# Kernel tuning notes

Hardware: AMD Instinct MI355X
Metric: run time of the kernel (lower is better)

The kernel has to match this reference:

```python
import jax, jax.numpy as jnp
import numpy as np


def fps(xyz, npoint):
    # farthest point sampling, starts at index 0 (matches pointnet2 CUDA kernel)
    B, N, _ = xyz.shape
    def step(carry, _):
        min_d, last = carry
        last_xyz = jnp.take_along_axis(xyz, last[:, None, None], axis=1)  # [B,1,3]
        d = jnp.sum((xyz - last_xyz) ** 2, axis=-1)                        # [B,N]
        min_d = jnp.minimum(min_d, d)
        nxt = jnp.argmax(min_d, axis=1).astype(jnp.int32)
        return (min_d, nxt), last
    init = (jnp.full((B, N), 1e10, xyz.dtype), jnp.zeros((B,), jnp.int32))
    _, idx = jax.lax.scan(step, init, None, length=npoint)
    return jnp.transpose(idx)  # [B, npoint]


def ball_query(xyz, new_xyz, radius, nsample):
    # first nsample points within radius; pad with first hit (0 if none) -- CUDA semantics
    N = xyz.shape[1]
    d2 = jnp.sum((new_xyz[:, :, None, :] - xyz[:, None, :, :]) ** 2, axis=-1)  # [B,S,N]
    cand = jnp.where(d2 < radius * radius, jnp.arange(N, dtype=jnp.int32)[None, None, :], N)
    srt = jnp.sort(cand, axis=-1)[..., :nsample]
    first = srt[..., :1]
    first = jnp.where(first == N, 0, first)
    return jnp.where(srt == N, first, srt)  # [B,S,K]


def gather_nbrs(x, idx):
    # x [B,N,C], idx [B,S,K] -> [B,S,K,C]
    B, S, K = idx.shape
    flat = jnp.take_along_axis(x, idx.reshape(B, S * K, 1), axis=1)
    return flat.reshape(B, S, K, x.shape[-1])


def shared_mlp(x, layers):
    # 1x1 conv (+ folded eval-mode BN) + ReLU per layer
    for w, b in layers:
        x = jax.nn.relu(jnp.einsum('bskc,oc->bsko', x, w) + b)
    return x


def sa_module(xyz, feat, npoint, radius, nsample, layers):
    idx = fps(xyz, npoint)
    new_xyz = jnp.take_along_axis(xyz, idx[:, :, None], axis=1)  # [B,S,3]
    gidx = ball_query(xyz, new_xyz, radius, nsample)
    grouped = gather_nbrs(xyz, gidx) - new_xyz[:, :, None, :]    # centered local xyz
    if feat is not None:
        grouped = jnp.concatenate([grouped, gather_nbrs(feat, gidx)], axis=-1)
    x = shared_mlp(grouped, layers)
    return new_xyz, jnp.max(x, axis=2)  # max-pool over neighbors -> [B,S,Cout]


def sa_module_all(xyz, feat, layers):
    # GroupAll: concat raw (uncentered) xyz with features, one group of all points
    x = jnp.concatenate([xyz, feat], axis=-1)[:, None]  # [B,1,N,3+C]
    x = shared_mlp(x, layers)
    return jnp.max(x, axis=2)[:, 0]  # [B,Cout]


def _forward(data, ws):
    B, T, N, _ = data.shape
    xyz = data.reshape(B * T, N, 3)
    xyz, feat = sa_module(xyz, None, 256, 0.2, 32, ws[0])
    xyz, feat = sa_module(xyz, feat, 128, 0.4, 32, ws[1])
    out = sa_module_all(xyz, feat, ws[2])
    return out.reshape(B, T, -1)


DIMS = [(3, 64), (64, 64), (64, 128), (131, 128), (128, 128), (128, 256), (259, 256), (256, 512), (512, 1024)]
NAMES = ['1_0', '1_1', '1_2', '2_0', '2_1', '2_2', '3_0', '3_1', '3_2']


def setup_inputs() -> dict:
    key = jax.random.key(0)
    keys = jax.random.split(key, 1 + 2 * len(DIMS))
    inp = {'data': jax.random.normal(keys[0], (4, 8, 4096, 3), jnp.float32)}
    for i, ((cin, cout), nm) in enumerate(zip(DIMS, NAMES)):
        inp['w' + nm] = jax.random.normal(keys[1 + 2 * i], (cout, cin), jnp.float32) / np.sqrt(cin).astype(np.float32)
        inp['b' + nm] = jax.random.normal(keys[2 + 2 * i], (cout,), jnp.float32) * 0.02
    return inp


def reference(data, w1_0, b1_0, w1_1, b1_1, w1_2, b1_2,
              w2_0, b2_0, w2_1, b2_1, w2_2, b2_2,
              w3_0, b3_0, w3_1, b3_1, w3_2, b3_2):
    ws = [[(w1_0, b1_0), (w1_1, b1_1), (w1_2, b1_2)],
          [(w2_0, b2_0), (w2_1, b2_1), (w2_2, b2_2)],
          [(w3_0, b3_0), (w3_1, b3_1), (w3_2, b3_2)]]
    return _forward(data, ws)
```

## Files before the change

kernel.cpp:

```cpp
#include <hip/hip_runtime.h>
#include <hip/hip_bf16.h>
#include <cstdint>
#include <cstddef>

#define BT 32
#define N1 4096
#define S1 256
#define S2 128
#define KNB 32

typedef __attribute__((ext_vector_type(8))) short short8;
typedef __attribute__((ext_vector_type(4))) float f32x4;

__device__ __forceinline__ float sqdist(float ax, float ay, float az,
                                        float bx, float by, float bz) {
    float dx = __fsub_rn(ax, bx), dy = __fsub_rn(ay, by), dz = __fsub_rn(az, bz);
    return __fadd_rn(__fadd_rn(__fmul_rn(dx, dx), __fmul_rn(dy, dy)), __fmul_rn(dz, dz));
}

__device__ __forceinline__ unsigned short f2bf(float f) {
    unsigned u = __float_as_uint(f);
    return (unsigned short)((u + 0x7FFFu + ((u >> 16) & 1u)) >> 16);
}
__device__ __forceinline__ float bf2f(unsigned short h) {
    return __uint_as_float(((unsigned)h) << 16);
}

__device__ __forceinline__ unsigned long long packvi(float v, int idx) {
    return ((unsigned long long)__float_as_uint(v) << 32) | (unsigned)(~idx);
}

template <int CTRL>
__device__ __forceinline__ unsigned long long dppmax(unsigned long long v) {
    int lo = (int)(unsigned)(v & 0xFFFFFFFFull);
    int hi = (int)(unsigned)(v >> 32);
    int lo2 = __builtin_amdgcn_update_dpp(0, lo, CTRL, 0xF, 0xF, false);
    int hi2 = __builtin_amdgcn_update_dpp(0, hi, CTRL, 0xF, 0xF, false);
    unsigned long long o = ((unsigned long long)(unsigned)hi2 << 32) | (unsigned)lo2;
    return o > v ? o : v;
}
#define ROR1 0x121
#define ROR2 0x122
#define ROR4 0x124
#define ROR8 0x128

__global__ __launch_bounds__(256) void fps1_kernel(const float* __restrict__ xyz,
                                                   float* __restrict__ nxz) {
    const int b = blockIdx.x, tid = threadIdx.x;
    const int lane = tid & 63, wv = tid >> 6;
    const float* X = xyz + (size_t)b * (N1 * 3);
    __shared__ float4 s4[N1];
    __shared__ unsigned long long slots[2][16];
    __shared__ float hist[S1 * 3];
    float px[16], py[16], pz[16], md[16];
    int bidx[16];
#pragma unroll
    for (int j = 0; j < 16; ++j) {
        int i = tid + 256 * j;
        float x = X[i * 3 + 0], y = X[i * 3 + 1], z = X[i * 3 + 2];
        s4[i] = make_float4(x, y, z, 0.f);
        px[j] = x; py[j] = y; pz[j] = z;
        md[j] = 1e10f;
        bidx[j] = i;
    }
    if (tid == 0) { hist[0] = X[0]; hist[1] = X[1]; hist[2] = X[2]; }
    __syncthreads();
    float4 c0 = s4[0];
    float lx = c0.x, ly = c0.y, lz = c0.z;
    for (int t = 1; t < S1; ++t) {
        float bv = -1.0f; int bi = 0;
#pragma unroll
        for (int j = 0; j < 16; ++j) {
            float d = sqdist(px[j], py[j], pz[j], lx, ly, lz);
            float m = fminf(md[j], d);
            md[j] = m;
            if (m > bv) { bv = m; bi = bidx[j]; }
        }
        unsigned long long best = packvi(bv, bi);
        best = dppmax<ROR1>(best);
        best = dppmax<ROR2>(best);
        best = dppmax<ROR4>(best);
        best = dppmax<ROR8>(best);
        if ((lane & 15) == 0) slots[t & 1][wv * 4 + (lane >> 4)] = best;
        __syncthreads();
        unsigned long long w = slots[t & 1][lane & 15];
        w = dppmax<ROR1>(w);
        w = dppmax<ROR2>(w);
        w = dppmax<ROR4>(w);
        w = dppmax<ROR8>(w);
        int vi = (int)(~(unsigned)w);
        float4 c = s4[vi];
        lx = c.x; ly = c.y; lz = c.z;
        if (tid == 0) { hist[t * 3 + 0] = lx; hist[t * 3 + 1] = ly; hist[t * 3 + 2] = lz; }
    }
    __syncthreads();
    for (int u = tid; u < S1 * 3; u += 256) nxz[(size_t)b * S1 * 3 + u] = hist[u];
}

__global__ __launch_bounds__(64) void fps2_kernel(const float* __restrict__ xyz1,
                                                  float* __restrict__ nxz2) {
    const int b = blockIdx.x, lane = threadIdx.x;
    const float* X = xyz1 + (size_t)b * (S1 * 3);
    __shared__ float4 s4[S1];
    float px[4], py[4], pz[4], md[4];
    int bidx[4];
#pragma unroll
    for (int j = 0; j < 4; ++j) {
        int i = lane + 64 * j;
        float x = X[i * 3 + 0], y = X[i * 3 + 1], z = X[i * 3 + 2];
        s4[i] = make_float4(x, y, z, 0.f);
        px[j] = x; py[j] = y; pz[j] = z;
        md[j] = 1e10f;
        bidx[j] = i;
    }
    if (lane == 0) {
        nxz2[(size_t)b * S2 * 3 + 0] = X[0];
        nxz2[(size_t)b * S2 * 3 + 1] = X[1];
        nxz2[(size_t)b * S2 * 3 + 2] = X[2];
    }
    float4 cc = s4[0];
    float lx = cc.x, ly = cc.y, lz = cc.z;
    for (int t = 1; t < S2; ++t) {
        float bv = -1.0f; int bi = 0;
#pragma unroll
        for (int j = 0; j < 4; ++j) {
            float d = sqdist(px[j], py[j], pz[j], lx, ly, lz);
            float m = fminf(md[j], d);
            md[j] = m;
            if (m > bv) { bv = m; bi = bidx[j]; }
        }
        unsigned long long best = packvi(bv, bi);
        best = dppmax<ROR1>(best);
        best = dppmax<ROR2>(best);
        best = dppmax<ROR4>(best);
        best = dppmax<ROR8>(best);
        { unsigned long long o = __shfl_xor(best, 16); best = o > best ? o : best; }
        { unsigned long long o = __shfl_xor(best, 32); best = o > best ? o : best; }
        int vi = (int)(~(unsigned)best);
        float4 c = s4[vi];
        lx = c.x; ly = c.y; lz = c.z;
        if (lane == 0) {
            float* dst = nxz2 + ((size_t)b * S2 + t) * 3;
            dst[0] = lx; dst[1] = ly; dst[2] = lz;
        }
    }
}

__global__ __launch_bounds__(256) void ballq1_kernel(const float* __restrict__ xyz,
                                                     const float* __restrict__ nxz,
                                                     int* __restrict__ gidx) {
    const int wid = (blockIdx.x * 256 + threadIdx.x) >> 6;
    const int lane = threadIdx.x & 63;
    const int b = wid >> 8;
    const float* X = xyz + (size_t)b * (N1 * 3);
    const float* C = nxz + (size_t)wid * 3;
    const float cx = C[0], cy = C[1], cz = C[2];
    const float r2 = (float)(0.2 * 0.2);
    int* G = gidx + (size_t)wid * KNB;
    int cnt = 0, first = 0;
    bool found = false;
    for (int j0 = 0; j0 < N1 && cnt < KNB; j0 += 64) {
        int j = j0 + lane;
        float d2 = sqdist(cx, cy, cz, X[j * 3 + 0], X[j * 3 + 1], X[j * 3 + 2]);
        bool hit = d2 < r2;
        unsigned long long mask = __ballot(hit);
        if (!found && mask) { first = j0 + __builtin_ctzll(mask); found = true; }
        if (hit) {
            int pos = cnt + __popcll(mask & ((1ull << lane) - 1ull));
            if (pos < KNB) G[pos] = j;
        }
        cnt += __popcll(mask);
    }
    if (cnt < KNB) {
        int pad = found ? first : 0;
        if (lane >= cnt && lane < KNB) G[lane] = pad;
    }
}

__global__ __launch_bounds__(256) void ballq2_kernel(const float* __restrict__ xyz1,
                                                     const float* __restrict__ nxz2,
                                                     int* __restrict__ gidx) {
    const int wid = (blockIdx.x * 256 + threadIdx.x) >> 6;
    const int lane = threadIdx.x & 63;
    const int b = wid >> 7;
    const float* X = xyz1 + (size_t)b * (S1 * 3);
    const float* C = nxz2 + (size_t)wid * 3;
    const float cx = C[0], cy = C[1], cz = C[2];
    const float r2 = (float)(0.4 * 0.4);
    int* G = gidx + (size_t)wid * KNB;
    int cnt = 0, first = 0;
    bool found = false;
    for (int j0 = 0; j0 < S1 && cnt < KNB; j0 += 64) {
        int j = j0 + lane;
        float d2 = sqdist(cx, cy, cz, X[j * 3 + 0], X[j * 3 + 1], X[j * 3 + 2]);
        bool hit = d2 < r2;
        unsigned long long mask = __ballot(hit);
        if (!found && mask) { first = j0 + __builtin_ctzll(mask); found = true; }
        if (hit) {
            int pos = cnt + __popcll(mask & ((1ull << lane) - 1ull));
            if (pos < KNB) G[pos] = j;
        }
        cnt += __popcll(mask);
    }
    if (cnt < KNB) {
        int pad = found ? first : 0;
        if (lane >= cnt && lane < KNB) G[lane] = pad;
    }
}

__global__ __launch_bounds__(256) void wconv_kernel(
    const float* __restrict__ w11, const float* __restrict__ w12,
    const float* __restrict__ w20, const float* __restrict__ w21,
    const float* __restrict__ w22, const float* __restrict__ w30,
    const float* __restrict__ w31, const float* __restrict__ w32,
    unsigned short* __restrict__ wb) {
    int u = blockIdx.x * 256 + threadIdx.x;
    if (u >= 823296) return;
    const float* src; int base, Kp, Ko; int perm = 0;
    if      (u < 4096)   { src = w11; base = 0;      Kp = 64;  Ko = 64;  }
    else if (u < 12288)  { src = w12; base = 4096;   Kp = 64;  Ko = 64;  }
    else if (u < 36864)  { src = w20; base = 12288;  Kp = 192; Ko = 131; perm = 128; }
    else if (u < 53248)  { src = w21; base = 36864;  Kp = 128; Ko = 128; }
    else if (u < 86016)  { src = w22; base = 53248;  Kp = 128; Ko = 128; }
    else if (u < 167936) { src = w30; base = 86016;  Kp = 320; Ko = 259; perm = 256; }
    else if (u < 299008) { src = w31; base = 167936; Kp = 256; Ko = 256; }
    else                 { src = w32; base = 299008; Kp = 512; Ko = 512; }
    int local = u - base;
    int n = local / Kp, k = local - n * Kp;
    float v;
    if (perm) {
        int ksrc = (k < perm) ? (k + 3) : ((k < perm + 3) ? (k - perm) : -1);
        v = (ksrc >= 0) ? src[(size_t)n * Ko + ksrc] : 0.f;
    } else {
        v = (k < Ko) ? src[(size_t)n * Ko + k] : 0.f;
    }
    wb[u] = f2bf(v);
}

__global__ __launch_bounds__(256) void m1_kernel(
    const float* __restrict__ xyz, const float* __restrict__ nxz,
    const int* __restrict__ g1,
    const float* __restrict__ w10, const float* __restrict__ b10,
    const unsigned short* __restrict__ w11b, const float* __restrict__ b11,
    const unsigned short* __restrict__ w12b, const float* __restrict__ b12,
    unsigned short* __restrict__ f1) {
    constexpr int AP = 72;
    __shared__ __align__(16) unsigned short As[128 * AP];
    __shared__ __align__(16) unsigned short Hs[128 * AP];
    __shared__ __align__(16) unsigned short Bs[128 * AP];
    __shared__ float sxyz[128 * 3];
    const int t = threadIdx.x;
    const int lane = t & 63, w = t >> 6;
    const int r16 = lane & 15, q = lane >> 4;
    const int m0 = blockIdx.x * 128;

    if (t < 128) {
        int row = m0 + t, bs = row >> 5, b = bs >> 8, j = g1[row];
        const float* P = xyz + ((size_t)b * N1 + j) * 3;
        const float* Cc = nxz + (size_t)bs * 3;
        sxyz[t * 3 + 0] = P[0] - Cc[0];
        sxyz[t * 3 + 1] = P[1] - Cc[1];
        sxyz[t * 3 + 2] = P[2] - Cc[2];
    }
    for (int c = t; c < 64 * 8; c += 256) {
        int row = c >> 3, ch = c & 7;
        *(short8*)&Bs[row * AP + ch * 8] = *(const short8*)&w11b[row * 64 + ch * 8];
    }
    __syncthreads();
    {
        const int r = t >> 1, half = (t & 1) * 32;
        const float x = sxyz[r * 3 + 0], y = sxyz[r * 3 + 1], z = sxyz[r * 3 + 2];
        unsigned short tmp[32];
#pragma unroll
        for (int o = 0; o < 32; ++o) {
            int oo = half + o;
            float acc = b10[oo];
            acc = fmaf(x, w10[oo * 3 + 0], acc);
            acc = fmaf(y, w10[oo * 3 + 1], acc);
            acc = fmaf(z, w10[oo * 3 + 2], acc);
            tmp[o] = f2bf(fmaxf(acc, 0.f));
        }
#pragma unroll
        for (int c2 = 0; c2 < 4; ++c2)
            *(short8*)&As[r * AP + half + c2 * 8] = *(short8*)&tmp[c2 * 8];
    }
    __syncthreads();
    {
        f32x4 acc[2][4];
#pragma unroll
        for (int i = 0; i < 2; ++i)
#pragma unroll
            for (int j = 0; j < 4; ++j) acc[i][j] = (f32x4){0.f, 0.f, 0.f, 0.f};
#pragma unroll
        for (int kk = 0; kk < 64; kk += 32) {
            short8 a0 = *(const short8*)&As[(w * 32 + r16) * AP + kk + q * 8];
            short8 a1 = *(const short8*)&As[(w * 32 + 16 + r16) * AP + kk + q * 8];
#pragma unroll
            for (int j = 0; j < 4; ++j) {
                short8 bf = *(const short8*)&Bs[(j * 16 + r16) * AP + kk + q * 8];
                acc[0][j] = __builtin_amdgcn_mfma_f32_16x16x32_bf16(a0, bf, acc[0][j], 0, 0, 0);
                acc[1][j] = __builtin_amdgcn_mfma_f32_16x16x32_bf16(a1, bf, acc[1][j], 0, 0, 0);
            }
        }
#pragma unroll
        for (int i = 0; i < 2; ++i)
#pragma unroll
            for (int j = 0; j < 4; ++j) {
                int col = j * 16 + r16;
                float bv = b11[col];
#pragma unroll
                for (int r = 0; r < 4; ++r) {
                    int row = w * 32 + i * 16 + q * 4 + r;
                    Hs[row * AP + col] = f2bf(fmaxf(acc[i][j][r] + bv, 0.f));
                }
            }
    }
    __syncthreads();
    for (int c = t; c < 128 * 8; c += 256) {
        int row = c >> 3, ch = c & 7;
        *(short8*)&Bs[row * AP + ch * 8] = *(const short8*)&w12b[row * 64 + ch * 8];
    }
    __syncthreads();
    {
        f32x4 acc[2][8];
#pragma unroll
        for (int i = 0; i < 2; ++i)
#pragma unroll
            for (int j = 0; j < 8; ++j) acc[i][j] = (f32x4){0.f, 0.f, 0.f, 0.f};
#pragma unroll
        for (int kk = 0; kk < 64; kk += 32) {
            short8 a0 = *(const short8*)&Hs[(w * 32 + r16) * AP + kk + q * 8];
            short8 a1 = *(const short8*)&Hs[(w * 32 + 16 + r16) * AP + kk + q * 8];
#pragma unroll
            for (int j = 0; j < 8; ++j) {
                short8 bf = *(const short8*)&Bs[(j * 16 + r16) * AP + kk + q * 8];
                acc[0][j] = __builtin_amdgcn_mfma_f32_16x16x32_bf16(a0, bf, acc[0][j], 0, 0, 0);
                acc[1][j] = __builtin_amdgcn_mfma_f32_16x16x32_bf16(a1, bf, acc[1][j], 0, 0, 0);
            }
        }
#pragma unroll
        for (int j = 0; j < 8; ++j) {
            int col = j * 16 + r16;
            float bv = b12[col];
            float mv = 0.f;
#pragma unroll
            for (int i = 0; i < 2; ++i)
#pragma unroll
                for (int r = 0; r < 4; ++r)
                    mv = fmaxf(mv, acc[i][j][r] + bv);
            mv = fmaxf(mv, __shfl_xor(mv, 16));
            mv = fmaxf(mv, __shfl_xor(mv, 32));
            if (q == 0)
                f1[(size_t)((m0 >> 5) + w) * 128 + col] = f2bf(mv);
        }
    }
}

__global__ __launch_bounds__(256) void m2_kernel(
    const float* __restrict__ xyz1, const float* __restrict__ nxz2,
    const int* __restrict__ g2, const unsigned short* __restrict__ f1,
    const unsigned short* __restrict__ w20p, const float* __restrict__ b20,
    const unsigned short* __restrict__ w21b, const float* __restrict__ b21,
    const unsigned short* __restrict__ w22b, const float* __restrict__ b22,
    unsigned short* __restrict__ f2) {
    constexpr int AP = 72, HP = 136;
    __shared__ __align__(16) unsigned short smem[36864];
    unsigned short* R1 = smem;
    unsigned short* R2 = smem + 18432;
    unsigned short* As = R1;
    unsigned short* Bs = R1 + 9216;
    unsigned short* H1 = R2;
    unsigned short* H2 = R1;
    unsigned short* Bs2 = R2;
    __shared__ int ribase[128];
    __shared__ unsigned short sxb[128 * 3];
    const int t = threadIdx.x;
    const int lane = t & 63, w = t >> 6;
    const int r16 = lane & 15, q = lane >> 4;
    const int m0 = blockIdx.x * 128;

    if (t < 128) {
        int row = m0 + t, bs = row >> 5, b = bs >> 7, j = g2[row];
        ribase[t] = (b * 256 + j) * 128;
        const float* P = xyz1 + ((size_t)b * S1 + j) * 3;
        const float* Cc = nxz2 + (size_t)bs * 3;
        sxb[t * 3 + 0] = f2bf(P[0] - Cc[0]);
        sxb[t * 3 + 1] = f2bf(P[1] - Cc[1]);
        sxb[t * 3 + 2] = f2bf(P[2] - Cc[2]);
    }
    __syncthreads();

    f32x4 acc[2][8];
#pragma unroll
    for (int i = 0; i < 2; ++i)
#pragma unroll
        for (int j = 0; j < 8; ++j) acc[i][j] = (f32x4){0.f, 0.f, 0.f, 0.f};
    for (int kt = 0; kt < 3; ++kt) {
        const int k0 = kt * 64;
        if (kt < 2) {
            for (int c = t; c < 128 * 8; c += 256) {
                int row = c >> 3, ch = c & 7;
                *(short8*)&As[row * AP + ch * 8] =
                    *(const short8*)&f1[(size_t)ribase[row] + k0 + ch * 8];
            }
        } else {
            for (int c = t; c < 128 * 8; c += 256) {
                int row = c >> 3, ch = c & 7;
                short8 v = (short8){0, 0, 0, 0, 0, 0, 0, 0};
                if (ch == 0) {
                    v[0] = (short)sxb[row * 3 + 0];
                    v[1] = (short)sxb[row * 3 + 1];
                    v[2] = (short)sxb[row * 3 + 2];
                }
                *(short8*)&As[row * AP + ch * 8] = v;
            }
        }
        for (int c = t; c < 128 * 8; c += 256) {
            int row = c >> 3, ch = c & 7;
            *(short8*)&Bs[row * AP + ch * 8] =
                *(const short8*)&w20p[(size_t)row * 192 + k0 + ch * 8];
        }
        __syncthreads();
#pragma unroll
        for (int kk = 0; kk < 64; kk += 32) {
            short8 a0 = *(const short8*)&As[(w * 32 + r16) * AP + kk + q * 8];
            short8 a1 = *(const short8*)&As[(w * 32 + 16 + r16) * AP + kk + q * 8];
#pragma unroll
            for (int j = 0; j < 8; ++j) {
                short8 bf = *(const short8*)&Bs[(j * 16 + r16) * AP + kk + q * 8];
                acc[0][j] = __builtin_amdgcn_mfma_f32_16x16x32_bf16(a0, bf, acc[0][j], 0, 0, 0);
                acc[1][j] = __builtin_amdgcn_mfma_f32_16x16x32_bf16(a1, bf, acc[1][j], 0, 0, 0);
            }
        }
        __syncthreads();
    }
#pragma unroll
    for (int i = 0; i < 2; ++i)
#pragma unroll
        for (int j = 0; j < 8; ++j) {
            int col = j * 16 + r16;
            float bv = b20[col];
#pragma unroll
            for (int r = 0; r < 4; ++r) {
                int row = w * 32 + i * 16 + q * 4 + r;
                H1[row * HP + col] = f2bf(fmaxf(acc[i][j][r] + bv, 0.f));
            }
        }
    __syncthreads();

#pragma unroll
    for (int i = 0; i < 2; ++i)
#pragma unroll
        for (int j = 0; j < 8; ++j) acc[i][j] = (f32x4){0.f, 0.f, 0.f, 0.f};
    for (int kt = 0; kt < 2; ++kt) {
        const int k0 = kt * 64;
        for (int c = t; c < 128 * 8; c += 256) {
            int row = c >> 3, ch = c & 7;
            *(short8*)&As[row * AP + ch * 8] =
                *(const short8*)&w21b[(size_t)row * 128 + k0 + ch * 8];
        }
        __syncthreads();
#pragma unroll
        for (int kk = 0; kk < 64; kk += 32) {
            short8 a0 = *(const short8*)&H1[(w * 32 + r16) * HP + k0 + kk + q * 8];
            short8 a1 = *(const short8*)&H1[(w * 32 + 16 + r16) * HP + k0 + kk + q * 8];
#pragma unroll
            for (int j = 0; j < 8; ++j) {
                short8 bf = *(const short8*)&As[(j * 16 + r16) * AP + kk + q * 8];
                acc[0][j] = __builtin_amdgcn_mfma_f32_16x16x32_bf16(a0, bf, acc[0][j], 0, 0, 0);
                acc[1][j] = __builtin_amdgcn_mfma_f32_16x16x32_bf16(a1, bf, acc[1][j], 0, 0, 0);
            }
        }
        __syncthreads();
    }
#pragma unroll
    for (int i = 0; i < 2; ++i)
#pragma unroll
        for (int j = 0; j < 8; ++j) {
            int col = j * 16 + r16;
            float bv = b21[col];
#pragma unroll
            for (int r = 0; r < 4; ++r) {
                int row = w * 32 + i * 16 + q * 4 + r;
                H2[row * HP + col] = f2bf(fmaxf(acc[i][j][r] + bv, 0.f));
            }
        }
    __syncthreads();

    f32x4 acc2[2][16];
#pragma unroll
    for (int i = 0; i < 2; ++i)
#pragma unroll
        for (int j = 0; j < 16; ++j) acc2[i][j] = (f32x4){0.f, 0.f, 0.f, 0.f};
    for (int kt = 0; kt < 2; ++kt) {
        const int k0 = kt * 64;
        for (int c = t; c < 256 * 8; c += 256) {
            int row = c >> 3, ch = c & 7;
            *(short8*)&Bs2[row * AP + ch * 8] =
                *(const short8*)&w22b[(size_t)row * 128 + k0 + ch * 8];
        }
        __syncthreads();
#pragma unroll
        for (int kk = 0; kk < 64; kk += 32) {
            short8 a0 = *(const short8*)&H2[(w * 32 + r16) * HP + k0 + kk + q * 8];
            short8 a1 = *(const short8*)&H2[(w * 32 + 16 + r16) * HP + k0 + kk + q * 8];
#pragma unroll
            for (int j = 0; j < 16; ++j) {
                short8 bf = *(const short8*)&Bs2[(j * 16 + r16) * AP + kk + q * 8];
                acc2[0][j] = __builtin_amdgcn_mfma_f32_16x16x32_bf16(a0, bf, acc2[0][j], 0, 0, 0);
                acc2[1][j] = __builtin_amdgcn_mfma_f32_16x16x32_bf16(a1, bf, acc2[1][j], 0, 0, 0);
            }
        }
        __syncthreads();
    }
#pragma unroll
    for (int j = 0; j < 16; ++j) {
        int col = j * 16 + r16;
        float bv = b22[col];
        float mv = 0.f;
#pragma unroll
        for (int i = 0; i < 2; ++i)
#pragma unroll
            for (int r = 0; r < 4; ++r)
                mv = fmaxf(mv, acc2[i][j][r] + bv);
        mv = fmaxf(mv, __shfl_xor(mv, 16));
        mv = fmaxf(mv, __shfl_xor(mv, 32));
        if (q == 0)
            f2[(size_t)((m0 >> 5) + w) * 256 + col] = f2bf(mv);
    }
}

__global__ __launch_bounds__(256) void l30_kernel(
    const float* __restrict__ nxz2, const unsigned short* __restrict__ f2,
    const unsigned short* __restrict__ w30p, const float* __restrict__ bias,
    unsigned short* __restrict__ C) {
    constexpr int AP = 72;
    __shared__ __align__(16) unsigned short As[128 * AP];
    __shared__ __align__(16) unsigned short Bs[128 * AP];
    const int t = threadIdx.x;
    const int lane = t & 63, w = t >> 6;
    const int r16 = lane & 15, q = lane >> 4;
    const int m0 = blockIdx.x * 128;
    const int n0 = blockIdx.y * 128;

    f32x4 acc[2][8];
#pragma unroll
    for (int i = 0; i < 2; ++i)
#pragma unroll
        for (int j = 0; j < 8; ++j) acc[i][j] = (f32x4){0.f, 0.f, 0.f, 0.f};

    for (int kt = 0; kt < 5; ++kt) {
        const int k0 = kt * 64;
        if (kt < 4) {
            for (int c = t; c < 128 * 8; c += 256) {
                int row = c >> 3, ch = c & 7;
                *(short8*)&As[row * AP + ch * 8] =
                    *(const short8*)&f2[(size_t)(m0 + row) * 256 + k0 + ch * 8];
            }
        } else {
            for (int c = t; c < 128 * 8; c += 256) {
                int row = c >> 3, ch = c & 7;
                short8 v = (short8){0, 0, 0, 0, 0, 0, 0, 0};
                if (ch == 0) {
                    const float* P = nxz2 + (size_t)(m0 + row) * 3;
                    v[0] = (short)f2bf(P[0]);
                    v[1] = (short)f2bf(P[1]);
                    v[2] = (short)f2bf(P[2]);
                }
                *(short8*)&As[row * AP + ch * 8] = v;
            }
        }
        for (int c = t; c < 128 * 8; c += 256) {
            int row = c >> 3, ch = c & 7;
            *(short8*)&Bs[row * AP + ch * 8] =
                *(const short8*)&w30p[(size_t)(n0 + row) * 320 + k0 + ch * 8];
        }
        __syncthreads();
#pragma unroll
        for (int kk = 0; kk < 64; kk += 32) {
            short8 a0 = *(const short8*)&As[(w * 32 + r16) * AP + kk + q * 8];
            short8 a1 = *(const short8*)&As[(w * 32 + 16 + r16) * AP + kk + q * 8];
#pragma unroll
            for (int j = 0; j < 8; ++j) {
                short8 bf = *(const short8*)&Bs[(j * 16 + r16) * AP + kk + q * 8];
                acc[0][j] = __builtin_amdgcn_mfma_f32_16x16x32_bf16(a0, bf, acc[0][j], 0, 0, 0);
                acc[1][j] = __builtin_amdgcn_mfma_f32_16x16x32_bf16(a1, bf, acc[1][j], 0, 0, 0);
            }
        }
        __syncthreads();
    }
#pragma unroll
    for (int i = 0; i < 2; ++i)
#pragma unroll
        for (int j = 0; j < 8; ++j) {
            int col = n0 + j * 16 + r16;
            float bv = bias[col];
#pragma unroll
            for (int r = 0; r < 4; ++r) {
                int row = m0 + w * 32 + i * 16 + q * 4 + r;
                C[(size_t)row * 256 + col] = f2bf(fmaxf(acc[i][j][r] + bv, 0.f));
            }
        }
}

template <int BN, bool POOL>
__global__ __launch_bounds__(256) void mfma_gemm(const unsigned short* __restrict__ X,
                                                 const unsigned short* __restrict__ W,
                                                 const float* __restrict__ bias,
                                                 unsigned short* __restrict__ C,
                                                 int M, int N, int K) {
    constexpr int BM = 128, BK = 64;
    constexpr int AP = BK + 8;
    constexpr int NT = BN / 16;
    __shared__ __align__(16) unsigned short As[BM * AP];
    __shared__ __align__(16) unsigned short Bs[BN * AP];
    const int t = threadIdx.x;
    const int lane = t & 63, w = t >> 6;
    const int m0 = blockIdx.x * BM;
    const int n0 = blockIdx.y * BN;
    const int r16 = lane & 15, q = lane >> 4;

    f32x4 acc[2][NT];
#pragma unroll
    for (int i = 0; i < 2; ++i)
#pragma unroll
        for (int j = 0; j < NT; ++j) acc[i][j] = (f32x4){0.f, 0.f, 0.f, 0.f};

    for (int k0 = 0; k0 < K; k0 += BK) {
        for (int c = t; c < BM * (BK / 8); c += 256) {
            int row = c >> 3, ch = c & 7;
            *(short8*)&As[row * AP + ch * 8] =
                *(const short8*)&X[(size_t)(m0 + row) * K + k0 + ch * 8];
        }
        for (int c = t; c < BN * (BK / 8); c += 256) {
            int row = c >> 3, ch = c & 7;
            *(short8*)&Bs[row * AP + ch * 8] =
                *(const short8*)&W[(size_t)(n0 + row) * K + k0 + ch * 8];
        }
        __syncthreads();
#pragma unroll
        for (int kk = 0; kk < BK; kk += 32) {
            short8 a0 = *(const short8*)&As[(w * 32 + r16) * AP + kk + q * 8];
            short8 a1 = *(const short8*)&As[(w * 32 + 16 + r16) * AP + kk + q * 8];
#pragma unroll
            for (int j = 0; j < NT; ++j) {
                short8 bf = *(const short8*)&Bs[(j * 16 + r16) * AP + kk + q * 8];
                acc[0][j] = __builtin_amdgcn_mfma_f32_16x16x32_bf16(a0, bf, acc[0][j], 0, 0, 0);
                acc[1][j] = __builtin_amdgcn_mfma_f32_16x16x32_bf16(a1, bf, acc[1][j], 0, 0, 0);
            }
        }
        __syncthreads();
    }

    if (!POOL) {
#pragma unroll
        for (int i = 0; i < 2; ++i)
#pragma unroll
            for (int j = 0; j < NT; ++j) {
                int col = n0 + j * 16 + r16;
                float bv = bias[col];
#pragma unroll
                for (int r = 0; r < 4; ++r) {
                    int row = m0 + w * 32 + i * 16 + q * 4 + r;
                    C[(size_t)row * N + col] = f2bf(fmaxf(acc[i][j][r] + bv, 0.f));
                }
            }
    } else {
#pragma unroll
        for (int j = 0; j < NT; ++j) {
            int col = n0 + j * 16 + r16;
            float bv = bias[col];
            float mv = 0.f;
#pragma unroll
            for (int i = 0; i < 2; ++i)
#pragma unroll
                for (int r = 0; r < 4; ++r)
                    mv = fmaxf(mv, acc[i][j][r] + bv);
            mv = fmaxf(mv, __shfl_xor(mv, 16));
            mv = fmaxf(mv, __shfl_xor(mv, 32));
            if (q == 0)
                C[(size_t)((m0 >> 5) + w) * N + col] = f2bf(mv);
        }
    }
}

__global__ __launch_bounds__(256) void maxn_kernel(const unsigned short* __restrict__ h,
                                                   float* __restrict__ out) {
    int id = blockIdx.x * 256 + threadIdx.x;
    int o = id & 1023, b = id >> 10;
    const unsigned short* p = h + (size_t)b * 128 * 1024 + o;
    float m = 0.f;
    for (int n = 0; n < 128; ++n) m = fmaxf(m, bf2f(p[(size_t)n * 1024]));
    out[id] = m;
}

extern "C" void kernel_launch(void* const* d_in, const int* in_sizes, int n_in,
                              void* d_out, int out_size, void* d_ws, size_t ws_size,
                              hipStream_t stream) {
    const float* data = (const float*)d_in[0];
    const float* w10 = (const float*)d_in[1];  const float* b10 = (const float*)d_in[2];
    const float* w11 = (const float*)d_in[3];  const float* b11 = (const float*)d_in[4];
    const float* w12 = (const float*)d_in[5];  const float* b12 = (const float*)d_in[6];
    const float* w20 = (const float*)d_in[7];  const float* b20 = (const float*)d_in[8];
    const float* w21 = (const float*)d_in[9];  const float* b21 = (const float*)d_in[10];
    const float* w22 = (const float*)d_in[11]; const float* b22 = (const float*)d_in[12];
    const float* w30 = (const float*)d_in[13]; const float* b30 = (const float*)d_in[14];
    const float* w31 = (const float*)d_in[15]; const float* b31 = (const float*)d_in[16];
    const float* w32 = (const float*)d_in[17]; const float* b32 = (const float*)d_in[18];
    float* out = (float*)d_out;

    char* ws = (char*)d_ws;
    size_t off = 0;
    auto alloc = [&](size_t bytes) -> void* {
        void* p = ws + off;
        off += (bytes + 255) & ~(size_t)255;
        return p;
    };
    float* nxz1 = (float*)alloc((size_t)BT * S1 * 3 * 4);
    int*   g1   = (int*)  alloc((size_t)BT * S1 * KNB * 4);
    float* nxz2 = (float*)alloc((size_t)BT * S2 * 3 * 4);
    int*   g2   = (int*)  alloc((size_t)BT * S2 * KNB * 4);
    unsigned short* wb  = (unsigned short*)alloc((size_t)823296 * 2);
    unsigned short* f1  = (unsigned short*)alloc((size_t)8192 * 128 * 2);
    unsigned short* f2  = (unsigned short*)alloc((size_t)4096 * 256 * 2);
    unsigned short* C1  = (unsigned short*)alloc((size_t)4096 * 256 * 2);
    unsigned short* C2  = (unsigned short*)alloc((size_t)4096 * 512 * 2);
    unsigned short* C3  = (unsigned short*)alloc((size_t)4096 * 1024 * 2);

    const unsigned short* w11b = wb + 0;
    const unsigned short* w12b = wb + 4096;
    const unsigned short* w20p = wb + 12288;
    const unsigned short* w21b = wb + 36864;
    const unsigned short* w22b = wb + 53248;
    const unsigned short* w30p = wb + 86016;
    const unsigned short* w31b = wb + 167936;
    const unsigned short* w32b = wb + 299008;

    wconv_kernel<<<(823296 + 255) / 256, 256, 0, stream>>>(w11, w12, w20, w21, w22, w30, w31, w32, wb);

    fps1_kernel<<<BT, 256, 0, stream>>>(data, nxz1);
    ballq1_kernel<<<(BT * S1) / 4, 256, 0, stream>>>(data, nxz1, g1);
    m1_kernel<<<262144 / 128, 256, 0, stream>>>(data, nxz1, g1, w10, b10, w11b, b11, w12b, b12, f1);
    fps2_kernel<<<BT, 64, 0, stream>>>(nxz1, nxz2);
    ballq2_kernel<<<(BT * S2) / 4, 256, 0, stream>>>(nxz1, nxz2, g2);
    m2_kernel<<<131072 / 128, 256, 0, stream>>>(nxz1, nxz2, g2, f1, w20p, b20, w21b, b21, w22b, b22, f2);
    l30_kernel<<<dim3(4096 / 128, 2), 256, 0, stream>>>(nxz2, f2, w30p, b30, C1);
    mfma_gemm<128, false><<<dim3(4096 / 128, 4), 256, 0, stream>>>(C1, w31b, b31, C2, 4096, 512, 256);
    mfma_gemm<128, false><<<dim3(4096 / 128, 8), 256, 0, stream>>>(C2, w32b, b32, C3, 4096, 1024, 512);
    maxn_kernel<<<(BT * 1024) / 256, 256, 0, stream>>>(C3, out);
}
```

Baseline: 515.4 us.

## Fuse fps2 into fps1, carry coords in reduction, fuse final GEMM with max-pool

The first farthest-point-sampling kernel now runs the second-level sampling inside the same block from its shared-memory history, which removes a separate launch. Its cross-wave reduction carries the winning point's coordinates through the DPP steps, so the dependent shared-memory load after the barrier goes away. The last GEMM now max-pools over the 128 points in-block and writes fp32 output directly, which drops the 4096x1024 intermediate and the separate max kernel. The 512-wide GEMM uses 64-row tiles to launch more blocks. These add register pressure in the reduction and idle waves while wave 0 runs the second sampling.

```diff
diff --git a/kernel.cpp b/kernel.cpp
--- a/kernel.cpp
+++ b/kernel.cpp
@@ -39,19 +39,32 @@
     unsigned long long o = ((unsigned long long)(unsigned)hi2 << 32) | (unsigned)lo2;
     return o > v ? o : v;
 }
+template <int CTRL>
+__device__ __forceinline__ void redstep(unsigned long long& v, float& x, float& y, float& z) {
+    int lo2 = __builtin_amdgcn_update_dpp(0, (int)(unsigned)(v & 0xFFFFFFFFull), CTRL, 0xF, 0xF, false);
+    int hi2 = __builtin_amdgcn_update_dpp(0, (int)(unsigned)(v >> 32), CTRL, 0xF, 0xF, false);
+    int x2 = __builtin_amdgcn_update_dpp(0, __float_as_int(x), CTRL, 0xF, 0xF, false);
+    int y2 = __builtin_amdgcn_update_dpp(0, __float_as_int(y), CTRL, 0xF, 0xF, false);
+    int z2 = __builtin_amdgcn_update_dpp(0, __float_as_int(z), CTRL, 0xF, 0xF, false);
+    unsigned long long o = ((unsigned long long)(unsigned)hi2 << 32) | (unsigned)(unsigned)lo2;
+    if (o > v) { v = o; x = __int_as_float(x2); y = __int_as_float(y2); z = __int_as_float(z2); }
+}
 #define ROR1 0x121
 #define ROR2 0x122
 #define ROR4 0x124
 #define ROR8 0x128
 
 __global__ __launch_bounds__(256) void fps1_kernel(const float* __restrict__ xyz,
-                                                   float* __restrict__ nxz) {
+                                                   float* __restrict__ nxz,
+                                                   float* __restrict__ nxz2) {
     const int b = blockIdx.x, tid = threadIdx.x;
     const int lane = tid & 63, wv = tid >> 6;
     const float* X = xyz + (size_t)b * (N1 * 3);
     __shared__ float4 s4[N1];
-    __shared__ unsigned long long slots[2][16];
+    __shared__ unsigned long long slots_v[2][16];
+    __shared__ float4 slots_c[2][16];
     __shared__ float hist[S1 * 3];
+    __shared__ float4 shist[S1];
     float px[16], py[16], pz[16], md[16];
     int bidx[16];
 #pragma unroll
@@ -65,8 +78,7 @@
     }
     if (tid == 0) { hist[0] = X[0]; hist[1] = X[1]; hist[2] = X[2]; }
     __syncthreads();
-    float4 c0 = s4[0];
-    float lx = c0.x, ly = c0.y, lz = c0.z;
+    float lx = X[0], ly = X[1], lz = X[2];
     for (int t = 1; t < S1; ++t) {
         float bv = -1.0f; int bi = 0;
 #pragma unroll
@@ -81,67 +93,65 @@
         best = dppmax<ROR2>(best);
         best = dppmax<ROR4>(best);
         best = dppmax<ROR8>(best);
-        if ((lane & 15) == 0) slots[t & 1][wv * 4 + (lane >> 4)] = best;
-        __syncthreads();
-        unsigned long long w = slots[t & 1][lane & 15];
-        w = dppmax<ROR1>(w);
-        w = dppmax<ROR2>(w);
-        w = dppmax<ROR4>(w);
-        w = dppmax<ROR8>(w);
-        int vi = (int)(~(unsigned)w);
-        float4 c = s4[vi];
-        lx = c.x; ly = c.y; lz = c.z;
+        if ((lane & 15) == 0) {
+            int vi = (int)(~(unsigned)best);
+            slots_v[t & 1][wv * 4 + (lane >> 4)] = best;
+            slots_c[t & 1][wv * 4 + (lane >> 4)] = s4[vi];
+        }
+        __syncthreads();
+        unsigned long long v = slots_v[t & 1][lane & 15];
+        float4 c = slots_c[t & 1][lane & 15];
+        float x = c.x, y = c.y, z = c.z;
+        redstep<ROR1>(v, x, y, z);
+        redstep<ROR2>(v, x, y, z);
+        redstep<ROR4>(v, x, y, z);
+        redstep<ROR8>(v, x, y, z);
+        lx = x; ly = y; lz = z;
         if (tid == 0) { hist[t * 3 + 0] = lx; hist[t * 3 + 1] = ly; hist[t * 3 + 2] = lz; }
     }
     __syncthreads();
     for (int u = tid; u < S1 * 3; u += 256) nxz[(size_t)b * S1 * 3 + u] = hist[u];
-}
-
-__global__ __launch_bounds__(64) void fps2_kernel(const float* __restrict__ xyz1,
-                                                  float* __restrict__ nxz2) {
-    const int b = blockIdx.x, lane = threadIdx.x;
-    const float* X = xyz1 + (size_t)b * (S1 * 3);
-    __shared__ float4 s4[S1];
-    float px[4], py[4], pz[4], md[4];
-    int bidx[4];
-#pragma unroll
-    for (int j = 0; j < 4; ++j) {
-        int i = lane + 64 * j;
-        float x = X[i * 3 + 0], y = X[i * 3 + 1], z = X[i * 3 + 2];
-        s4[i] = make_float4(x, y, z, 0.f);
-        px[j] = x; py[j] = y; pz[j] = z;
-        md[j] = 1e10f;
-        bidx[j] = i;
-    }
-    if (lane == 0) {
-        nxz2[(size_t)b * S2 * 3 + 0] = X[0];
-        nxz2[(size_t)b * S2 * 3 + 1] = X[1];
-        nxz2[(size_t)b * S2 * 3 + 2] = X[2];
-    }
-    float4 cc = s4[0];
-    float lx = cc.x, ly = cc.y, lz = cc.z;
-    for (int t = 1; t < S2; ++t) {
-        float bv = -1.0f; int bi = 0;
+    if (wv == 0) {
+        float p2x[4], p2y[4], p2z[4], m2[4];
+        int b2i[4];
 #pragma unroll
         for (int j = 0; j < 4; ++j) {
-            float d = sqdist(px[j], py[j], pz[j], lx, ly, lz);
-            float m = fminf(md[j], d);
-            md[j] = m;
-            if (m > bv) { bv = m; bi = bidx[j]; }
-        }
-        unsigned long long best = packvi(bv, bi);
-        best = dppmax<ROR1>(best);
-        best = dppmax<ROR2>(best);
-        best = dppmax<ROR4>(best);
-        best = dppmax<ROR8>(best);
-        { unsigned long long o = __shfl_xor(best, 16); best = o > best ? o : best; }
-        { unsigned long long o = __shfl_xor(best, 32); best = o > best ? o : best; }
-        int vi = (int)(~(unsigned)best);
-        float4 c = s4[vi];
-        lx = c.x; ly = c.y; lz = c.z;
+            int i = lane + 64 * j;
+            float x = hist[i * 3 + 0], y = hist[i * 3 + 1], z = hist[i * 3 + 2];
+            shist[i] = make_float4(x, y, z, 0.f);
+            p2x[j] = x; p2y[j] = y; p2z[j] = z;
+            m2[j] = 1e10f;
+            b2i[j] = i;
+        }
         if (lane == 0) {
-            float* dst = nxz2 + ((size_t)b * S2 + t) * 3;
-            dst[0] = lx; dst[1] = ly; dst[2] = lz;
+            nxz2[(size_t)b * S2 * 3 + 0] = hist[0];
+            nxz2[(size_t)b * S2 * 3 + 1] = hist[1];
+            nxz2[(size_t)b * S2 * 3 + 2] = hist[2];
+        }
+        float cx = hist[0], cy = hist[1], cz = hist[2];
+        for (int t = 1; t < S2; ++t) {
+            float bv = -1.0f; int bi = 0;
+#pragma unroll
+            for (int j = 0; j < 4; ++j) {
+                float d = sqdist(p2x[j], p2y[j], p2z[j], cx, cy, cz);
+                float m = fminf(m2[j], d);
+                m2[j] = m;
+                if (m > bv) { bv = m; bi = b2i[j]; }
+            }
+            unsigned long long best = packvi(bv, bi);
+            best = dppmax<ROR1>(best);
+            best = dppmax<ROR2>(best);
+            best = dppmax<ROR4>(best);
+            best = dppmax<ROR8>(best);
+            { unsigned long long o = __shfl_xor(best, 16); best = o > best ? o : best; }
+            { unsigned long long o = __shfl_xor(best, 32); best = o > best ? o : best; }
+            int vi = (int)(~(unsigned)best);
+            float4 c = shist[vi];
+            cx = c.x; cy = c.y; cz = c.z;
+            if (lane == 0) {
+                float* dst = nxz2 + ((size_t)b * S2 + t) * 3;
+                dst[0] = cx; dst[1] = cy; dst[2] = cz;
+            }
         }
     }
 }
@@ -603,36 +613,36 @@
         }
 }
 
-template <int BN, bool POOL>
+template <int BM_>
 __global__ __launch_bounds__(256) void mfma_gemm(const unsigned short* __restrict__ X,
                                                  const unsigned short* __restrict__ W,
                                                  const float* __restrict__ bias,
                                                  unsigned short* __restrict__ C,
                                                  int M, int N, int K) {
-    constexpr int BM = 128, BK = 64;
-    constexpr int AP = BK + 8;
-    constexpr int NT = BN / 16;
-    __shared__ __align__(16) unsigned short As[BM * AP];
-    __shared__ __align__(16) unsigned short Bs[BN * AP];
+    constexpr int BK = 64, AP = BK + 8;
+    constexpr int RW = BM_ / 64;
+    constexpr int WR = BM_ / 4;
+    __shared__ __align__(16) unsigned short As[BM_ * AP];
+    __shared__ __align__(16) unsigned short Bs[128 * AP];
     const int t = threadIdx.x;
     const int lane = t & 63, w = t >> 6;
-    const int m0 = blockIdx.x * BM;
-    const int n0 = blockIdx.y * BN;
+    const int m0 = blockIdx.x * BM_;
+    const int n0 = blockIdx.y * 128;
     const int r16 = lane & 15, q = lane >> 4;
 
-    f32x4 acc[2][NT];
-#pragma unroll
-    for (int i = 0; i < 2; ++i)
-#pragma unroll
-        for (int j = 0; j < NT; ++j) acc[i][j] = (f32x4){0.f, 0.f, 0.f, 0.f};
+    f32x4 acc[RW][8];
+#pragma unroll
+    for (int i = 0; i < RW; ++i)
+#pragma unroll
+        for (int j = 0; j < 8; ++j) acc[i][j] = (f32x4){0.f, 0.f, 0.f, 0.f};
 
     for (int k0 = 0; k0 < K; k0 += BK) {
-        for (int c = t; c < BM * (BK / 8); c += 256) {
+        for (int c = t; c < BM_ * 8; c += 256) {
             int row = c >> 3, ch = c & 7;
             *(short8*)&As[row * AP + ch * 8] =
                 *(const short8*)&X[(size_t)(m0 + row) * K + k0 + ch * 8];
         }
-        for (int c = t; c < BN * (BK / 8); c += 256) {
+        for (int c = t; c < 128 * 8; c += 256) {
             int row = c >> 3, ch = c & 7;
             *(short8*)&Bs[row * AP + ch * 8] =
                 *(const short8*)&W[(size_t)(n0 + row) * K + k0 + ch * 8];
@@ -640,10 +650,72 @@
         __syncthreads();
 #pragma unroll
         for (int kk = 0; kk < BK; kk += 32) {
+            short8 a[RW];
+#pragma unroll
+            for (int i = 0; i < RW; ++i)
+                a[i] = *(const short8*)&As[(w * WR + i * 16 + r16) * AP + kk + q * 8];
+#pragma unroll
+            for (int j = 0; j < 8; ++j) {
+                short8 bf = *(const short8*)&Bs[(j * 16 + r16) * AP + kk + q * 8];
+#pragma unroll
+                for (int i = 0; i < RW; ++i)
+                    acc[i][j] = __builtin_amdgcn_mfma_f32_16x16x32_bf16(a[i], bf, acc[i][j], 0, 0, 0);
+            }
+        }
+        __syncthreads();
+    }
+#pragma unroll
+    for (int i = 0; i < RW; ++i)
+#pragma unroll
+        for (int j = 0; j < 8; ++j) {
+            int col = n0 + j * 16 + r16;
+            float bv = bias[col];
+#pragma unroll
+            for (int r = 0; r < 4; ++r) {
+                int row = m0 + w * WR + i * 16 + q * 4 + r;
+                C[(size_t)row * N + col] = f2bf(fmaxf(acc[i][j][r] + bv, 0.f));
+            }
+        }
+}
+
+__global__ __launch_bounds__(256) void gemm_pool128(const unsigned short* __restrict__ X,
+                                                    const unsigned short* __restrict__ W,
+                                                    const float* __restrict__ bias,
+                                                    float* __restrict__ out) {
+    constexpr int BK = 64, AP = BK + 8, K = 512;
+    __shared__ __align__(16) unsigned short As[128 * AP];
+    __shared__ __align__(16) unsigned short Bs[128 * AP];
+    __shared__ float pool[4][128];
+    const int t = threadIdx.x;
+    const int lane = t & 63, w = t >> 6;
+    const int m0 = blockIdx.x * 128;
+    const int n0 = blockIdx.y * 128;
+    const int r16 = lane & 15, q = lane >> 4;
+
+    f32x4 acc[2][8];
+#pragma unroll
+    for (int i = 0; i < 2; ++i)
+#pragma unroll
+        for (int j = 0; j < 8; ++j) acc[i][j] = (f32x4){0.f, 0.f, 0.f, 0.f};
+
+    for (int k0 = 0; k0 < K; k0 += BK) {
+        for (int c = t; c < 128 * 8; c += 256) {
+            int row = c >> 3, ch = c & 7;
+            *(short8*)&As[row * AP + ch * 8] =
+                *(const short8*)&X[(size_t)(m0 + row) * K + k0 + ch * 8];
+        }
+        for (int c = t; c < 128 * 8; c += 256) {
+            int row = c >> 3, ch = c & 7;
+            *(short8*)&Bs[row * AP + ch * 8] =
+                *(const short8*)&W[(size_t)(n0 + row) * K + k0 + ch * 8];
+        }
+        __syncthreads();
+#pragma unroll
+        for (int kk = 0; kk < BK; kk += 32) {
             short8 a0 = *(const short8*)&As[(w * 32 + r16) * AP + kk + q * 8];
             short8 a1 = *(const short8*)&As[(w * 32 + 16 + r16) * AP + kk + q * 8];
 #pragma unroll
-            for (int j = 0; j < NT; ++j) {
+            for (int j = 0; j < 8; ++j) {
                 short8 bf = *(const short8*)&Bs[(j * 16 + r16) * AP + kk + q * 8];
                 acc[0][j] = __builtin_amdgcn_mfma_f32_16x16x32_bf16(a0, bf, acc[0][j], 0, 0, 0);
                 acc[1][j] = __builtin_amdgcn_mfma_f32_16x16x32_bf16(a1, bf, acc[1][j], 0, 0, 0);
@@ -651,47 +723,24 @@
         }
         __syncthreads();
     }
-
-    if (!POOL) {
+#pragma unroll
+    for (int j = 0; j < 8; ++j) {
+        float bv = bias[n0 + j * 16 + r16];
+        float mv = 0.f;
 #pragma unroll
         for (int i = 0; i < 2; ++i)
 #pragma unroll
-            for (int j = 0; j < NT; ++j) {
-                int col = n0 + j * 16 + r16;
-                float bv = bias[col];
-#pragma unroll
-                for (int r = 0; r < 4; ++r) {
-                    int row = m0 + w * 32 + i * 16 + q * 4 + r;
-                    C[(size_t)row * N + col] = f2bf(fmaxf(acc[i][j][r] + bv, 0.f));
-                }
-            }
-    } else {
-#pragma unroll
-        for (int j = 0; j < NT; ++j) {
-            int col = n0 + j * 16 + r16;
-            float bv = bias[col];
-            float mv = 0.f;
-#pragma unroll
-            for (int i = 0; i < 2; ++i)
-#pragma unroll
-                for (int r = 0; r < 4; ++r)
-                    mv = fmaxf(mv, acc[i][j][r] + bv);
-            mv = fmaxf(mv, __shfl_xor(mv, 16));
-            mv = fmaxf(mv, __shfl_xor(mv, 32));
-            if (q == 0)
-                C[(size_t)((m0 >> 5) + w) * N + col] = f2bf(mv);
-        }
-    }
-}
-
-__global__ __launch_bounds__(256) void maxn_kernel(const unsigned short* __restrict__ h,
-                                                   float* __restrict__ out) {
-    int id = blockIdx.x * 256 + threadIdx.x;
-    int o = id & 1023, b = id >> 10;
-    const unsigned short* p = h + (size_t)b * 128 * 1024 + o;
-    float m = 0.f;
-    for (int n = 0; n < 128; ++n) m = fmaxf(m, bf2f(p[(size_t)n * 1024]));
-    out[id] = m;
+            for (int r = 0; r < 4; ++r)
+                mv = fmaxf(mv, acc[i][j][r] + bv);
+        mv = fmaxf(mv, __shfl_xor(mv, 16));
+        mv = fmaxf(mv, __shfl_xor(mv, 32));
+        if (q == 0) pool[w][j * 16 + r16] = mv;
+    }
+    __syncthreads();
+    if (t < 128) {
+        float m = fmaxf(fmaxf(pool[0][t], pool[1][t]), fmaxf(pool[2][t], pool[3][t]));
+        out[(size_t)blockIdx.x * 1024 + n0 + t] = m;
+    }
 }
 
 extern "C" void kernel_launch(void* const* d_in, const int* in_sizes, int n_in,
@@ -725,7 +774,6 @@
     unsigned short* f2  = (unsigned short*)alloc((size_t)4096 * 256 * 2);
     unsigned short* C1  = (unsigned short*)alloc((size_t)4096 * 256 * 2);
     unsigned short* C2  = (unsigned short*)alloc((size_t)4096 * 512 * 2);
-    unsigned short* C3  = (unsigned short*)alloc((size_t)4096 * 1024 * 2);
 
     const unsigned short* w11b = wb + 0;
     const unsigned short* w12b = wb + 4096;
@@ -738,14 +786,12 @@
 
     wconv_kernel<<<(823296 + 255) / 256, 256, 0, stream>>>(w11, w12, w20, w21, w22, w30, w31, w32, wb);
 
-    fps1_kernel<<<BT, 256, 0, stream>>>(data, nxz1);
+    fps1_kernel<<<BT, 256, 0, stream>>>(data, nxz1, nxz2);
     ballq1_kernel<<<(BT * S1) / 4, 256, 0, stream>>>(data, nxz1, g1);
     m1_kernel<<<262144 / 128, 256, 0, stream>>>(data, nxz1, g1, w10, b10, w11b, b11, w12b, b12, f1);
-    fps2_kernel<<<BT, 64, 0, stream>>>(nxz1, nxz2);
     ballq2_kernel<<<(BT * S2) / 4, 256, 0, stream>>>(nxz1, nxz2, g2);
     m2_kernel<<<131072 / 128, 256, 0, stream>>>(nxz1, nxz2, g2, f1, w20p, b20, w21b, b21, w22b, b22, f2);
     l30_kernel<<<dim3(4096 / 128, 2), 256, 0, stream>>>(nxz2, f2, w30p, b30, C1);
-    mfma_gemm<128, false><<<dim3(4096 / 128, 4), 256, 0, stream>>>(C1, w31b, b31, C2, 4096, 512, 256);
-    mfma_gemm<128, false><<<dim3(4096 / 128, 8), 256, 0, stream>>>(C2, w32b, b32, C3, 4096, 1024, 512);
-    maxn_kernel<<<(BT * 1024) / 256, 256, 0, stream>>>(C3, out);
-}
+    mfma_gemm<64><<<dim3(4096 / 64, 4), 256, 0, stream>>>(C1, w31b, b31, C2, 4096, 512, 256);
+    gemm_pool128<<<dim3(4096 / 128, 8), 256, 0, stream>>>(C2, w32b, b32, out);
+}
```

After: 512.9 us. About the same (-0.5%).
